# Kernel optimization log

Measured on AMD Instinct MI355X. Metric: run time of the kernel, lower is better.

## Reference

```python
import jax, jax.numpy as jnp
import numpy as np

H = 128          # h_dim
N_NODES = 100000
N_EDGES = 1600000
N_GRAPHS = 256
EPS_BN = 1e-5


def setup_inputs() -> dict:
    key = jax.random.key(0)
    ks = jax.random.split(key, 12)
    x = jax.random.normal(ks[0], (N_NODES, 4), dtype=jnp.float32)
    edge_index = jax.random.randint(ks[1], (2, N_EDGES), 0, N_NODES, dtype=jnp.int64)
    batch = jnp.sort(jax.random.randint(ks[2], (N_NODES,), 0, N_GRAPHS, dtype=jnp.int64))
    # Linear weights (xavier-ish scale), stored as [in, out]
    W1 = jax.random.normal(ks[3], (4, H), dtype=jnp.float32) * (1.0 / np.sqrt(4))
    W2 = jax.random.normal(ks[4], (H, H), dtype=jnp.float32) * (1.0 / np.sqrt(H))
    W3 = jax.random.normal(ks[5], (H, H), dtype=jnp.float32) * (1.0 / np.sqrt(H))
    Wfc = jax.random.normal(ks[6], (H, 1), dtype=jnp.float32) * (1.0 / np.sqrt(H))
    def bn_params(k):
        k1, k2, k3, k4 = jax.random.split(k, 4)
        gamma = 1.0 + 0.1 * jax.random.normal(k1, (H,), dtype=jnp.float32)
        beta = 0.1 * jax.random.normal(k2, (H,), dtype=jnp.float32)
        mean = 0.1 * jax.random.normal(k3, (H,), dtype=jnp.float32)
        var = 1.0 + 0.1 * jax.random.uniform(k4, (H,), dtype=jnp.float32)
        return gamma, beta, mean, var
    g1, b1, m1, v1 = bn_params(ks[7])
    g2, b2, m2, v2 = bn_params(ks[8])
    g3, b3, m3, v3 = bn_params(ks[9])
    return {
        "x": x, "edge_index": edge_index, "batch": batch,
        "W1": W1, "g1": g1, "b1": b1, "m1": m1, "v1": v1,
        "W2": W2, "g2": g2, "b2": b2, "m2": m2, "v2": v2,
        "W3": W3, "g3": g3, "b3": b3, "m3": m3, "v3": v3,
        "Wfc": Wfc,
    }


def _gin_layer(h, src, dst, W, gamma, beta, mean, var):
    # GINConv with eps=0: mlp(x + sum_{j in N(i)} x_j)
    aggr = jax.ops.segment_sum(h[src], dst, num_segments=N_NODES)
    z = (h + aggr) @ W                                  # Linear(bias=False)
    z = (z - mean) * (gamma / jnp.sqrt(var + EPS_BN)) + beta  # BatchNorm1d (eval)
    return jax.nn.relu(z)


def reference(x, edge_index, batch,
              W1, g1, b1, m1, v1,
              W2, g2, b2, m2, v2,
              W3, g3, b3, m3, v3,
              Wfc):
    src, dst = edge_index[0], edge_index[1]
    h = _gin_layer(x, src, dst, W1, g1, b1, m1, v1)
    h = _gin_layer(h, src, dst, W2, g2, b2, m2, v2)
    h = _gin_layer(h, src, dst, W3, g3, b3, m3, v3)
    # dropout: identity in eval mode
    sums = jax.ops.segment_sum(h, batch, num_segments=N_GRAPHS)      # [G, H]
    cnts = jax.ops.segment_sum(jnp.ones((N_NODES, 1), h.dtype), batch,
                               num_segments=N_GRAPHS)                # [G, 1]
    pooled = sums / jnp.maximum(cnts, 1.0)
    return jax.nn.sigmoid(pooled @ Wfc)                               # [G, 1]
```

## Files before the change

kernel.cpp:

```cpp
#include <hip/hip_runtime.h>
#include <hip/hip_fp8.h>
#include <math.h>

#define N_NODES 100000
#define N_EDGES 1600000
#define N_GRAPHS 256
#define H 128
#define EPS_BN 1e-5f
#define ELLW 64

#define PSZ 256
#define PSH 8
#define P_PART 391
#define BLD_NBLK 200
#define EPT 32
#define EPB_A (256 * EPT)

typedef unsigned int uint;
typedef unsigned short ushort;
typedef __attribute__((ext_vector_type(8))) short bf16x8;
typedef __attribute__((ext_vector_type(4))) float f32x4;
typedef __attribute__((ext_vector_type(2))) float f32x2;
typedef __attribute__((ext_vector_type(4))) int i32x4;

__device__ __forceinline__ uint f2bf_bits(float x) {
    uint u = __float_as_uint(x);
    return (u + 0x7fffu + ((u >> 16) & 1u)) >> 16;
}
__device__ __forceinline__ uint pack_bf2(float a, float b) {
    return f2bf_bits(a) | (f2bf_bits(b) << 16);
}

__device__ __forceinline__ unsigned char f32_to_fp8(float x) {
#if __has_builtin(__builtin_amdgcn_cvt_pk_fp8_f32)
    int v = __builtin_amdgcn_cvt_pk_fp8_f32(x, 0.0f, 0, false);
    return (unsigned char)(v & 0xff);
#else
    __hip_fp8_e4m3 q(x);
    return (unsigned char)q.__x;
#endif
}
__device__ __forceinline__ f32x4 fp8x4_to_f32x4(uint v) {
    f32x4 r;
#if __has_builtin(__builtin_amdgcn_cvt_pk_f32_fp8)
    f32x2 lo = __builtin_amdgcn_cvt_pk_f32_fp8((int)v, false);
    f32x2 hi = __builtin_amdgcn_cvt_pk_f32_fp8((int)v, true);
    r.x = lo.x; r.y = lo.y; r.z = hi.x; r.w = hi.y;
#else
    __hip_fp8_e4m3 a, b, c, d;
    a.__x = (unsigned char)(v & 0xff);
    b.__x = (unsigned char)((v >> 8) & 0xff);
    c.__x = (unsigned char)((v >> 16) & 0xff);
    d.__x = (unsigned char)((v >> 24) & 0xff);
    r.x = (float)a; r.y = (float)b; r.z = (float)c; r.w = (float)d;
#endif
    return r;
}

__global__ __launch_bounds__(256) void k_hist(const int* __restrict__ dst,
                                              int* __restrict__ hist,
                                              const int* __restrict__ batch,
                                              int* __restrict__ gstart,
                                              const float* __restrict__ W2,
                                              ushort* __restrict__ Wpk2,
                                              const float* __restrict__ W3,
                                              ushort* __restrict__ Wpk3,
                                              float* __restrict__ Gz) {
    __shared__ int h[P_PART];
    int b = blockIdx.x;
    if (b < BLD_NBLK) {
        for (int i = threadIdx.x; i < P_PART; i += 256) h[i] = 0;
        __syncthreads();
        int base = b * EPB_A + threadIdx.x * EPT;
        #pragma unroll
        for (int j = 0; j < EPT / 4; j++) {
            int e = base + j * 4;
            if (e + 4 <= N_EDGES) {
                i32x4 d = __builtin_nontemporal_load((const i32x4*)&dst[e]);
                atomicAdd(&h[d.x >> PSH], 1);
                atomicAdd(&h[d.y >> PSH], 1);
                atomicAdd(&h[d.z >> PSH], 1);
                atomicAdd(&h[d.w >> PSH], 1);
            }
        }
        __syncthreads();
        for (int i = threadIdx.x; i < P_PART; i += 256)
            hist[b * P_PART + i] = h[i];
        return;
    }
    if (b < 592) {
        int n = (b - 200) * 256 + threadIdx.x;
        if (n >= N_NODES) return;
        int g = batch[n];
        int gp = (n == 0) ? -1 : batch[n - 1];
        for (int gr = gp + 1; gr <= g; gr++) gstart[gr] = n;
        if (n == N_NODES - 1) {
            for (int gr = g + 1; gr <= N_GRAPHS; gr++) gstart[gr] = N_NODES;
        }
        return;
    }
    if (b >= 608) {
        if (threadIdx.x < N_GRAPHS) Gz[threadIdx.x] = 0.0f;
        return;
    }
    const float* W = (b < 600) ? W2 : W3;
    ushort* Wpk = (b < 600) ? Wpk2 : Wpk3;
    int t = ((b < 600) ? (b - 592) : (b - 600)) * 256 + threadIdx.x;
    int lane = t & 63, nt = (t >> 6) & 7, kt = t >> 9;
    int n = nt * 16 + (lane & 15);
    int kbase = kt * 32 + (lane >> 4) * 8;
    ushort v[8];
    #pragma unroll
    for (int j = 0; j < 8; j++)
        v[j] = (ushort)f2bf_bits(W[(size_t)(kbase + j) * H + n]);
    uint4 pk;
    pk.x = (uint)v[0] | ((uint)v[1] << 16);
    pk.y = (uint)v[2] | ((uint)v[3] << 16);
    pk.z = (uint)v[4] | ((uint)v[5] << 16);
    pk.w = (uint)v[6] | ((uint)v[7] << 16);
    *(uint4*)&Wpk[(size_t)t * 8] = pk;
}

__global__ __launch_bounds__(256) void k_scan_a(const int* __restrict__ hist,
                                                int* __restrict__ offs,
                                                int* __restrict__ tot) {
    __shared__ int lds[256];
    int p = blockIdx.x;
    int t = threadIdx.x;
    int v = (t < BLD_NBLK) ? hist[t * P_PART + p] : 0;
    lds[t] = v;
    __syncthreads();
    for (int off = 1; off < 256; off <<= 1) {
        int tmp = (t >= off) ? lds[t - off] : 0;
        __syncthreads();
        lds[t] += tmp;
        __syncthreads();
    }
    if (t < BLD_NBLK) offs[t * P_PART + p] = lds[t] - v;
    if (t == 255) tot[p] = lds[255];
}

__global__ void k_scan_b(const int* __restrict__ tot, int* __restrict__ parr) {
    __shared__ int lds[512];
    int p = threadIdx.x;
    int v = (p < P_PART) ? tot[p] : 0;
    lds[p] = v;
    __syncthreads();
    for (int off = 1; off < 512; off <<= 1) {
        int tmp = (p >= off) ? lds[p - off] : 0;
        __syncthreads();
        lds[p] += tmp;
        __syncthreads();
    }
    if (p < P_PART) parr[p] = lds[p] - v;
    if (p == 0) parr[P_PART] = N_EDGES;
}

__global__ __launch_bounds__(256) void k_scatter(const int* __restrict__ src,
                                                 const int* __restrict__ dst,
                                                 const int* __restrict__ offs,
                                                 const int* __restrict__ parr,
                                                 uint* __restrict__ ebuf) {
    __shared__ int lofs[P_PART];
    for (int i = threadIdx.x; i < P_PART; i += 256)
        lofs[i] = offs[blockIdx.x * P_PART + i] + parr[i];
    __syncthreads();
    int base = blockIdx.x * EPB_A + threadIdx.x * EPT;
    #pragma unroll
    for (int j = 0; j < EPT / 4; j++) {
        int e = base + j * 4;
        if (e + 4 <= N_EDGES) {
            i32x4 d = __builtin_nontemporal_load((const i32x4*)&dst[e]);
            i32x4 s = __builtin_nontemporal_load((const i32x4*)&src[e]);
            #pragma unroll
            for (int k = 0; k < 4; k++) {
                int dk = (k == 0) ? d.x : (k == 1) ? d.y : (k == 2) ? d.z : d.w;
                int sk = (k == 0) ? s.x : (k == 1) ? s.y : (k == 2) ? s.z : s.w;
                int pos = atomicAdd(&lofs[dk >> PSH], 1);
                ebuf[pos] = (uint)sk | ((uint)(dk & (PSZ - 1)) << 24);
            }
        }
    }
}

__global__ __launch_bounds__(256) void k_build(const uint* __restrict__ ebuf,
                                               const int* __restrict__ parr,
                                               int* __restrict__ cnt,
                                               int* __restrict__ ell) {
    __shared__ int lc[PSZ];
    int p = blockIdx.x;
    for (int i = threadIdx.x; i < PSZ; i += 256) lc[i] = 0;
    __syncthreads();
    int e0 = parr[p], e1 = parr[p + 1];
    for (int i = e0 + threadIdx.x; i < e1; i += 256) {
        uint v = __builtin_nontemporal_load(&ebuf[i]);
        int dl = (int)(v >> 24);
        int slot = atomicAdd(&lc[dl], 1);
        if (slot < ELLW)
            ell[(size_t)(p * PSZ + dl) * ELLW + slot] = (int)(v & 0x00FFFFFFu);
    }
    __syncthreads();
    int nb = p * PSZ;
    for (int i = threadIdx.x; i < PSZ; i += 256) {
        int n = nb + i;
        if (n < N_NODES) cnt[n] = lc[i];
    }
}

__global__ __launch_bounds__(256) void k_layer1(
    const float* __restrict__ x, const int* __restrict__ cnt,
    const int* __restrict__ ell, const float* __restrict__ W1,
    const float* __restrict__ gamma, const float* __restrict__ beta,
    const float* __restrict__ mean, const float* __restrict__ var,
    uint* __restrict__ Hf8) {
    __shared__ float scs[128], shs[128];
    int tid = threadIdx.x;
    if (tid < 128) {
        float sc = gamma[tid] * rsqrtf(var[tid] + EPS_BN);
        scs[tid] = sc;
        shs[tid] = beta[tid] - mean[tid] * sc;
    }
    __syncthreads();
    int lane = tid & 63, wave = tid >> 6;
    int sub = lane >> 4, m = lane & 15;
    int n = blockIdx.x * 16 + wave * 4 + sub;
    if (n >= N_NODES) return;
    int cn = cnt[n]; if (cn > ELLW) cn = ELLW;
    const int* row = &ell[(size_t)n * ELLW];
    float4 acc = {0.f, 0.f, 0.f, 0.f};
    for (int e = m; e < cn; e += 16) {
        float4 v = *(const float4*)&x[(size_t)row[e] * 4];
        acc.x += v.x; acc.y += v.y; acc.z += v.z; acc.w += v.w;
    }
    #pragma unroll
    for (int off = 8; off > 0; off >>= 1) {
        acc.x += __shfl_down(acc.x, off, 16);
        acc.y += __shfl_down(acc.y, off, 16);
        acc.z += __shfl_down(acc.z, off, 16);
        acc.w += __shfl_down(acc.w, off, 16);
    }
    int src = lane & 48;
    float4 xs = *(const float4*)&x[(size_t)n * 4];
    float uu[4];
    uu[0] = __shfl(acc.x, src, 64) + xs.x;
    uu[1] = __shfl(acc.y, src, 64) + xs.y;
    uu[2] = __shfl(acc.z, src, 64) + xs.z;
    uu[3] = __shfl(acc.w, src, 64) + xs.w;
    int j0 = m * 8;
    float z[8] = {0.f, 0.f, 0.f, 0.f, 0.f, 0.f, 0.f, 0.f};
    #pragma unroll
    for (int k = 0; k < 4; k++) {
        float4 wa = *(const float4*)&W1[k * H + j0];
        float4 wb = *(const float4*)&W1[k * H + j0 + 4];
        z[0] += uu[k] * wa.x; z[1] += uu[k] * wa.y;
        z[2] += uu[k] * wa.z; z[3] += uu[k] * wa.w;
        z[4] += uu[k] * wb.x; z[5] += uu[k] * wb.y;
        z[6] += uu[k] * wb.z; z[7] += uu[k] * wb.w;
    }
    #pragma unroll
    for (int i = 0; i < 8; i++)
        z[i] = fmaxf(z[i] * scs[j0 + i] + shs[j0 + i], 0.0f);
    uint2 q;
    q.x = (uint)f32_to_fp8(z[0]) | ((uint)f32_to_fp8(z[1]) << 8)
        | ((uint)f32_to_fp8(z[2]) << 16) | ((uint)f32_to_fp8(z[3]) << 24);
    q.y = (uint)f32_to_fp8(z[4]) | ((uint)f32_to_fp8(z[5]) << 8)
        | ((uint)f32_to_fp8(z[6]) << 16) | ((uint)f32_to_fp8(z[7]) << 24);
    *(uint2*)&Hf8[(size_t)n * 32 + m * 2] = q;
}

__global__ __launch_bounds__(256) void k_aggr128(
    const uint* __restrict__ Hf8, const int* __restrict__ cnt,
    const int* __restrict__ ell, uint* __restrict__ Ubf) {
    int t = blockIdx.x * 256 + threadIdx.x;
    int n = t >> 6, lane = t & 63;
    if (n >= N_NODES) return;
    int half = lane >> 5, c4 = lane & 31;
    float a0 = 0.f, a1 = 0.f, a2 = 0.f, a3 = 0.f;
    int cn = cnt[n]; if (cn > ELLW) cn = ELLW;
    const int* row = &ell[(size_t)n * ELLW];
    int e = half;
    for (; e + 14 < cn; e += 16) {
        int s0 = row[e + 0], s1 = row[e + 2], s2 = row[e + 4], s3 = row[e + 6];
        int s4 = row[e + 8], s5 = row[e + 10], s6 = row[e + 12], s7 = row[e + 14];
        uint p0 = Hf8[(size_t)s0 * 32 + c4];
        uint p1 = Hf8[(size_t)s1 * 32 + c4];
        uint p2 = Hf8[(size_t)s2 * 32 + c4];
        uint p3 = Hf8[(size_t)s3 * 32 + c4];
        uint p4 = Hf8[(size_t)s4 * 32 + c4];
        uint p5 = Hf8[(size_t)s5 * 32 + c4];
        uint p6 = Hf8[(size_t)s6 * 32 + c4];
        uint p7 = Hf8[(size_t)s7 * 32 + c4];
        f32x4 f0 = fp8x4_to_f32x4(p0), f1 = fp8x4_to_f32x4(p1);
        f32x4 f2 = fp8x4_to_f32x4(p2), f3 = fp8x4_to_f32x4(p3);
        f32x4 f4 = fp8x4_to_f32x4(p4), f5 = fp8x4_to_f32x4(p5);
        f32x4 f6 = fp8x4_to_f32x4(p6), f7 = fp8x4_to_f32x4(p7);
        a0 += (f0.x + f1.x + f2.x + f3.x) + (f4.x + f5.x + f6.x + f7.x);
        a1 += (f0.y + f1.y + f2.y + f3.y) + (f4.y + f5.y + f6.y + f7.y);
        a2 += (f0.z + f1.z + f2.z + f3.z) + (f4.z + f5.z + f6.z + f7.z);
        a3 += (f0.w + f1.w + f2.w + f3.w) + (f4.w + f5.w + f6.w + f7.w);
    }
    for (; e + 6 < cn; e += 8) {
        int s0 = row[e + 0], s1 = row[e + 2], s2 = row[e + 4], s3 = row[e + 6];
        uint p0 = Hf8[(size_t)s0 * 32 + c4];
        uint p1 = Hf8[(size_t)s1 * 32 + c4];
        uint p2 = Hf8[(size_t)s2 * 32 + c4];
        uint p3 = Hf8[(size_t)s3 * 32 + c4];
        f32x4 f0 = fp8x4_to_f32x4(p0), f1 = fp8x4_to_f32x4(p1);
        f32x4 f2 = fp8x4_to_f32x4(p2), f3 = fp8x4_to_f32x4(p3);
        a0 += f0.x + f1.x + f2.x + f3.x;
        a1 += f0.y + f1.y + f2.y + f3.y;
        a2 += f0.z + f1.z + f2.z + f3.z;
        a3 += f0.w + f1.w + f2.w + f3.w;
    }
    for (; e < cn; e += 2) {
        f32x4 f = fp8x4_to_f32x4(Hf8[(size_t)row[e] * 32 + c4]);
        a0 += f.x; a1 += f.y; a2 += f.z; a3 += f.w;
    }
    a0 += __shfl_down(a0, 32, 64);
    a1 += __shfl_down(a1, 32, 64);
    a2 += __shfl_down(a2, 32, 64);
    a3 += __shfl_down(a3, 32, 64);
    if (half == 0) {
        f32x4 sf = fp8x4_to_f32x4(Hf8[(size_t)n * 32 + c4]);
        a0 += sf.x; a1 += sf.y; a2 += sf.z; a3 += sf.w;
        uint2 ov; ov.x = pack_bf2(a0, a1); ov.y = pack_bf2(a2, a3);
        *(uint2*)&Ubf[(size_t)n * 64 + c4 * 2] = ov;
    }
}

__global__ __launch_bounds__(256) void k_gemm_mfma(
    const uint* __restrict__ Ubf, const uint* __restrict__ Wpk,
    const float* __restrict__ gamma, const float* __restrict__ beta,
    const float* __restrict__ mean, const float* __restrict__ var,
    unsigned char* __restrict__ Hf8,
    const int* __restrict__ batch, const float* __restrict__ Wfc,
    float* __restrict__ Gz, int mode) {
    __shared__ uint lds_u[64 * 68];
    __shared__ float wfc[128];
    __shared__ int bb[64];
    __shared__ float sblk[64];
    int tid = threadIdx.x;
    int row0 = blockIdx.x * 64;
    if (mode == 2) {
        if (tid < 128) wfc[tid] = Wfc[tid];
        if (tid < 64) {
            int rr = row0 + tid;
            bb[tid] = (rr < N_NODES) ? batch[rr] : -1;
        }
    }
    #pragma unroll
    for (int it = 0; it < 4; it++) {
        int r = it * 16 + (tid >> 4);
        int c = (tid & 15) * 4;
        int gr = row0 + r; if (gr >= N_NODES) gr = N_NODES - 1;
        uint4 v = *(const uint4*)&Ubf[(size_t)gr * 64 + c];
        *(uint4*)&lds_u[r * 68 + c] = v;
    }
    __syncthreads();

    int wave = tid >> 6, lane = tid & 63;
    int m = lane & 15, quad = lane >> 4;
    bf16x8 a[4];
    #pragma unroll
    for (int kt = 0; kt < 4; kt++)
        a[kt] = *(const bf16x8*)&lds_u[(wave * 16 + m) * 68 + kt * 16 + quad * 4];

    f32x4 acc[8];
    #pragma unroll
    for (int nt = 0; nt < 8; nt++) acc[nt] = (f32x4){0.f, 0.f, 0.f, 0.f};

    #pragma unroll
    for (int nt = 0; nt < 8; nt++) {
        #pragma unroll
        for (int kt = 0; kt < 4; kt++) {
            bf16x8 b = *(const bf16x8*)&Wpk[((size_t)(kt * 8 + nt) * 64 + lane) * 4];
            acc[nt] = __builtin_amdgcn_mfma_f32_16x16x32_bf16(a[kt], b, acc[nt], 0, 0, 0);
        }
    }

    if (mode == 1) {
        #pragma unroll
        for (int nt = 0; nt < 8; nt++) {
            int col = nt * 16 + m;
            float sc = gamma[col] * rsqrtf(var[col] + EPS_BN);
            float sh = beta[col] - mean[col] * sc;
            #pragma unroll
            for (int r = 0; r < 4; r++) {
                int row = row0 + wave * 16 + quad * 4 + r;
                float z = fmaxf(acc[nt][r] * sc + sh, 0.0f);
                uint b8 = (uint)f32_to_fp8(z);
                uint b8n = __shfl_down(b8, 1, 64);
                if ((m & 1) == 0 && row < N_NODES) {
                    *(ushort*)&Hf8[(size_t)row * 128 + col] =
                        (ushort)(b8 | (b8n << 8));
                }
            }
        }
    } else {
        float pr[4] = {0.f, 0.f, 0.f, 0.f};
        #pragma unroll
        for (int nt = 0; nt < 8; nt++) {
            int col = nt * 16 + m;
            float sc = gamma[col] * rsqrtf(var[col] + EPS_BN);
            float sh = beta[col] - mean[col] * sc;
            float wf = wfc[col];
            #pragma unroll
            for (int r = 0; r < 4; r++) {
                float z = fmaxf(acc[nt][r] * sc + sh, 0.0f);
                pr[r] += z * wf;
            }
        }
        #pragma unroll
        for (int r = 0; r < 4; r++) {
            float p = pr[r];
            p += __shfl_down(p, 8, 16);
            p += __shfl_down(p, 4, 16);
            p += __shfl_down(p, 2, 16);
            p += __shfl_down(p, 1, 16);
            if (m == 0) sblk[wave * 16 + quad * 4 + r] = p;
        }
        __syncthreads();
        if (tid == 0) {
            int i = 0;
            while (i < 64 && row0 + i < N_NODES) {
                int g = bb[i];
                float s = 0.0f;
                while (i < 64 && row0 + i < N_NODES && bb[i] == g) {
                    s += sblk[i]; i++;
                }
                atomicAdd(&Gz[g], s);
            }
        }
    }
}

__global__ void k_fc(const float* __restrict__ Gz, const int* __restrict__ gstart,
                     float* __restrict__ out) {
    int g = threadIdx.x;
    if (g < N_GRAPHS) {
        int c = gstart[g + 1] - gstart[g];
        float z = Gz[g] / fmaxf((float)c, 1.0f);
        out[g] = 1.0f / (1.0f + expf(-z));
    }
}

extern "C" void kernel_launch(void* const* d_in, const int* in_sizes, int n_in,
                              void* d_out, int out_size, void* d_ws, size_t ws_size,
                              hipStream_t stream) {
    const float* x     = (const float*)d_in[0];
    const int*   ei    = (const int*)d_in[1];
    const int*   batch = (const int*)d_in[2];
    const float* W1    = (const float*)d_in[3];
    const float* g1    = (const float*)d_in[4];
    const float* b1    = (const float*)d_in[5];
    const float* m1    = (const float*)d_in[6];
    const float* v1    = (const float*)d_in[7];
    const float* W2    = (const float*)d_in[8];
    const float* g2    = (const float*)d_in[9];
    const float* b2    = (const float*)d_in[10];
    const float* m2    = (const float*)d_in[11];
    const float* v2    = (const float*)d_in[12];
    const float* W3    = (const float*)d_in[13];
    const float* g3    = (const float*)d_in[14];
    const float* b3    = (const float*)d_in[15];
    const float* m3    = (const float*)d_in[16];
    const float* v3    = (const float*)d_in[17];
    const float* Wfc   = (const float*)d_in[18];
    float* out = (float*)d_out;

    const int* srcp = ei;
    const int* dstp = ei + N_EDGES;

    uint* Ubf  = (uint*)d_ws;
    uint* Hf8a = Ubf + (size_t)N_NODES * 64;
    uint* Hf8b = Hf8a + (size_t)N_NODES * 32;
    int* cnt   = (int*)(Hf8b + (size_t)N_NODES * 32);
    int* ell   = cnt + N_NODES;
    int* gstart = ell + (size_t)N_NODES * ELLW;
    ushort* Wpk2 = (ushort*)(gstart + 260);
    ushort* Wpk3 = Wpk2 + 16384;
    int* hist  = (int*)(Wpk3 + 16384);
    int* offs  = hist + BLD_NBLK * P_PART;
    int* parr  = offs + BLD_NBLK * P_PART;
    int* tot   = parr + 400;
    float* Gz  = (float*)(tot + 400);
    uint* ebuf = (uint*)Ubf;

    k_hist<<<609, 256, 0, stream>>>(dstp, hist, batch, gstart, W2, Wpk2, W3, Wpk3, Gz);
    k_scan_a<<<P_PART, 256, 0, stream>>>(hist, offs, tot);
    k_scan_b<<<1, 512, 0, stream>>>(tot, parr);
    k_scatter<<<BLD_NBLK, 256, 0, stream>>>(srcp, dstp, offs, parr, ebuf);
    k_build<<<P_PART, 256, 0, stream>>>(ebuf, parr, cnt, ell);

    k_layer1<<<(N_NODES + 15) / 16, 256, 0, stream>>>(
        x, cnt, ell, W1, g1, b1, m1, v1, Hf8a);
    k_aggr128<<<(N_NODES * 64 + 255) / 256, 256, 0, stream>>>(Hf8a, cnt, ell, Ubf);
    k_gemm_mfma<<<(N_NODES + 63) / 64, 256, 0, stream>>>(
        Ubf, (const uint*)Wpk2, g2, b2, m2, v2, (unsigned char*)Hf8b,
        batch, Wfc, Gz, 1);
    k_aggr128<<<(N_NODES * 64 + 255) / 256, 256, 0, stream>>>(Hf8b, cnt, ell, Ubf);
    k_gemm_mfma<<<(N_NODES + 63) / 64, 256, 0, stream>>>(
        Ubf, (const uint*)Wpk3, g3, b3, m3, v3, (unsigned char*)Hf8a,
        batch, Wfc, Gz, 2);
    k_fc<<<1, 256, 0, stream>>>(Gz, gstart, out);
}
```

Measured before the change: 310.6 us.

## Fold partition scan into scatter/build and widen aggregation loads to 8 bytes

```diff
diff --git a/kernel.cpp b/kernel.cpp
--- a/kernel.cpp
+++ b/kernel.cpp
@@ -140,32 +140,34 @@
     if (t == 255) tot[p] = lds[255];
 }
 
-__global__ void k_scan_b(const int* __restrict__ tot, int* __restrict__ parr) {
-    __shared__ int lds[512];
-    int p = threadIdx.x;
-    int v = (p < P_PART) ? tot[p] : 0;
-    lds[p] = v;
-    __syncthreads();
-    for (int off = 1; off < 512; off <<= 1) {
-        int tmp = (p >= off) ? lds[p - off] : 0;
-        __syncthreads();
-        lds[p] += tmp;
-        __syncthreads();
-    }
-    if (p < P_PART) parr[p] = lds[p] - v;
-    if (p == 0) parr[P_PART] = N_EDGES;
-}
-
 __global__ __launch_bounds__(256) void k_scatter(const int* __restrict__ src,
                                                  const int* __restrict__ dst,
                                                  const int* __restrict__ offs,
-                                                 const int* __restrict__ parr,
+                                                 const int* __restrict__ tot,
                                                  uint* __restrict__ ebuf) {
+    __shared__ int sparr[P_PART];
     __shared__ int lofs[P_PART];
-    for (int i = threadIdx.x; i < P_PART; i += 256)
-        lofs[i] = offs[blockIdx.x * P_PART + i] + parr[i];
-    __syncthreads();
-    int base = blockIdx.x * EPB_A + threadIdx.x * EPT;
+    int tid = threadIdx.x;
+    if (tid < 64) {
+        int running = 0;
+        for (int base = 0; base < P_PART; base += 64) {
+            int idx = base + tid;
+            int v = (idx < P_PART) ? tot[idx] : 0;
+            int s = v;
+            #pragma unroll
+            for (int off = 1; off < 64; off <<= 1) {
+                int u = __shfl_up(s, off, 64);
+                if (tid >= off) s += u;
+            }
+            if (idx < P_PART) sparr[idx] = running + s - v;
+            running += __shfl(s, 63, 64);
+        }
+    }
+    __syncthreads();
+    for (int i = tid; i < P_PART; i += 256)
+        lofs[i] = offs[blockIdx.x * P_PART + i] + sparr[i];
+    __syncthreads();
+    int base = blockIdx.x * EPB_A + tid * EPT;
     #pragma unroll
     for (int j = 0; j < EPT / 4; j++) {
         int e = base + j * 4;
@@ -184,15 +186,25 @@
 }
 
 __global__ __launch_bounds__(256) void k_build(const uint* __restrict__ ebuf,
-                                               const int* __restrict__ parr,
+                                               const int* __restrict__ tot,
                                                int* __restrict__ cnt,
                                                int* __restrict__ ell) {
     __shared__ int lc[PSZ];
+    __shared__ int red[256];
     int p = blockIdx.x;
-    for (int i = threadIdx.x; i < PSZ; i += 256) lc[i] = 0;
-    __syncthreads();
-    int e0 = parr[p], e1 = parr[p + 1];
-    for (int i = e0 + threadIdx.x; i < e1; i += 256) {
+    int tid = threadIdx.x;
+    int psum = 0;
+    for (int i = tid; i < p; i += 256) psum += tot[i];
+    red[tid] = psum;
+    for (int i = tid; i < PSZ; i += 256) lc[i] = 0;
+    __syncthreads();
+    for (int off = 128; off > 0; off >>= 1) {
+        if (tid < off) red[tid] += red[tid + off];
+        __syncthreads();
+    }
+    int e0 = red[0];
+    int e1 = e0 + tot[p];
+    for (int i = e0 + tid; i < e1; i += 256) {
         uint v = __builtin_nontemporal_load(&ebuf[i]);
         int dl = (int)(v >> 24);
         int slot = atomicAdd(&lc[dl], 1);
@@ -201,7 +213,7 @@
     }
     __syncthreads();
     int nb = p * PSZ;
-    for (int i = threadIdx.x; i < PSZ; i += 256) {
+    for (int i = tid; i < PSZ; i += 256) {
         int n = nb + i;
         if (n < N_NODES) cnt[n] = lc[i];
     }
@@ -269,62 +281,59 @@
 }
 
 __global__ __launch_bounds__(256) void k_aggr128(
-    const uint* __restrict__ Hf8, const int* __restrict__ cnt,
+    const uint2* __restrict__ Hf8, const int* __restrict__ cnt,
     const int* __restrict__ ell, uint* __restrict__ Ubf) {
     int t = blockIdx.x * 256 + threadIdx.x;
     int n = t >> 6, lane = t & 63;
     if (n >= N_NODES) return;
-    int half = lane >> 5, c4 = lane & 31;
+    int g = lane >> 4, c = lane & 15;
     float a0 = 0.f, a1 = 0.f, a2 = 0.f, a3 = 0.f;
+    float a4 = 0.f, a5 = 0.f, a6 = 0.f, a7 = 0.f;
     int cn = cnt[n]; if (cn > ELLW) cn = ELLW;
     const int* row = &ell[(size_t)n * ELLW];
-    int e = half;
-    for (; e + 14 < cn; e += 16) {
-        int s0 = row[e + 0], s1 = row[e + 2], s2 = row[e + 4], s3 = row[e + 6];
-        int s4 = row[e + 8], s5 = row[e + 10], s6 = row[e + 12], s7 = row[e + 14];
-        uint p0 = Hf8[(size_t)s0 * 32 + c4];
-        uint p1 = Hf8[(size_t)s1 * 32 + c4];
-        uint p2 = Hf8[(size_t)s2 * 32 + c4];
-        uint p3 = Hf8[(size_t)s3 * 32 + c4];
-        uint p4 = Hf8[(size_t)s4 * 32 + c4];
-        uint p5 = Hf8[(size_t)s5 * 32 + c4];
-        uint p6 = Hf8[(size_t)s6 * 32 + c4];
-        uint p7 = Hf8[(size_t)s7 * 32 + c4];
-        f32x4 f0 = fp8x4_to_f32x4(p0), f1 = fp8x4_to_f32x4(p1);
-        f32x4 f2 = fp8x4_to_f32x4(p2), f3 = fp8x4_to_f32x4(p3);
-        f32x4 f4 = fp8x4_to_f32x4(p4), f5 = fp8x4_to_f32x4(p5);
-        f32x4 f6 = fp8x4_to_f32x4(p6), f7 = fp8x4_to_f32x4(p7);
-        a0 += (f0.x + f1.x + f2.x + f3.x) + (f4.x + f5.x + f6.x + f7.x);
-        a1 += (f0.y + f1.y + f2.y + f3.y) + (f4.y + f5.y + f6.y + f7.y);
-        a2 += (f0.z + f1.z + f2.z + f3.z) + (f4.z + f5.z + f6.z + f7.z);
-        a3 += (f0.w + f1.w + f2.w + f3.w) + (f4.w + f5.w + f6.w + f7.w);
-    }
-    for (; e + 6 < cn; e += 8) {
-        int s0 = row[e + 0], s1 = row[e + 2], s2 = row[e + 4], s3 = row[e + 6];
-        uint p0 = Hf8[(size_t)s0 * 32 + c4];
-        uint p1 = Hf8[(size_t)s1 * 32 + c4];
-        uint p2 = Hf8[(size_t)s2 * 32 + c4];
-        uint p3 = Hf8[(size_t)s3 * 32 + c4];
-        f32x4 f0 = fp8x4_to_f32x4(p0), f1 = fp8x4_to_f32x4(p1);
-        f32x4 f2 = fp8x4_to_f32x4(p2), f3 = fp8x4_to_f32x4(p3);
-        a0 += f0.x + f1.x + f2.x + f3.x;
-        a1 += f0.y + f1.y + f2.y + f3.y;
-        a2 += f0.z + f1.z + f2.z + f3.z;
-        a3 += f0.w + f1.w + f2.w + f3.w;
-    }
-    for (; e < cn; e += 2) {
-        f32x4 f = fp8x4_to_f32x4(Hf8[(size_t)row[e] * 32 + c4]);
-        a0 += f.x; a1 += f.y; a2 += f.z; a3 += f.w;
-    }
-    a0 += __shfl_down(a0, 32, 64);
-    a1 += __shfl_down(a1, 32, 64);
-    a2 += __shfl_down(a2, 32, 64);
-    a3 += __shfl_down(a3, 32, 64);
-    if (half == 0) {
-        f32x4 sf = fp8x4_to_f32x4(Hf8[(size_t)n * 32 + c4]);
-        a0 += sf.x; a1 += sf.y; a2 += sf.z; a3 += sf.w;
-        uint2 ov; ov.x = pack_bf2(a0, a1); ov.y = pack_bf2(a2, a3);
-        *(uint2*)&Ubf[(size_t)n * 64 + c4 * 2] = ov;
+    int e = g;
+    for (; e + 12 < cn; e += 16) {
+        int s0 = row[e], s1 = row[e + 4], s2 = row[e + 8], s3 = row[e + 12];
+        uint2 p0 = Hf8[(size_t)s0 * 16 + c];
+        uint2 p1 = Hf8[(size_t)s1 * 16 + c];
+        uint2 p2 = Hf8[(size_t)s2 * 16 + c];
+        uint2 p3 = Hf8[(size_t)s3 * 16 + c];
+        f32x4 l0 = fp8x4_to_f32x4(p0.x), h0 = fp8x4_to_f32x4(p0.y);
+        f32x4 l1 = fp8x4_to_f32x4(p1.x), h1 = fp8x4_to_f32x4(p1.y);
+        f32x4 l2 = fp8x4_to_f32x4(p2.x), h2 = fp8x4_to_f32x4(p2.y);
+        f32x4 l3 = fp8x4_to_f32x4(p3.x), h3 = fp8x4_to_f32x4(p3.y);
+        a0 += l0.x + l1.x + l2.x + l3.x;
+        a1 += l0.y + l1.y + l2.y + l3.y;
+        a2 += l0.z + l1.z + l2.z + l3.z;
+        a3 += l0.w + l1.w + l2.w + l3.w;
+        a4 += h0.x + h1.x + h2.x + h3.x;
+        a5 += h0.y + h1.y + h2.y + h3.y;
+        a6 += h0.z + h1.z + h2.z + h3.z;
+        a7 += h0.w + h1.w + h2.w + h3.w;
+    }
+    for (; e < cn; e += 4) {
+        uint2 p = Hf8[(size_t)row[e] * 16 + c];
+        f32x4 lo = fp8x4_to_f32x4(p.x), hi = fp8x4_to_f32x4(p.y);
+        a0 += lo.x; a1 += lo.y; a2 += lo.z; a3 += lo.w;
+        a4 += hi.x; a5 += hi.y; a6 += hi.z; a7 += hi.w;
+    }
+    a0 += __shfl_down(a0, 32, 64); a1 += __shfl_down(a1, 32, 64);
+    a2 += __shfl_down(a2, 32, 64); a3 += __shfl_down(a3, 32, 64);
+    a4 += __shfl_down(a4, 32, 64); a5 += __shfl_down(a5, 32, 64);
+    a6 += __shfl_down(a6, 32, 64); a7 += __shfl_down(a7, 32, 64);
+    a0 += __shfl_down(a0, 16, 64); a1 += __shfl_down(a1, 16, 64);
+    a2 += __shfl_down(a2, 16, 64); a3 += __shfl_down(a3, 16, 64);
+    a4 += __shfl_down(a4, 16, 64); a5 += __shfl_down(a5, 16, 64);
+    a6 += __shfl_down(a6, 16, 64); a7 += __shfl_down(a7, 16, 64);
+    if (g == 0) {
+        uint2 sp = Hf8[(size_t)n * 16 + c];
+        f32x4 slo = fp8x4_to_f32x4(sp.x), shi = fp8x4_to_f32x4(sp.y);
+        a0 += slo.x; a1 += slo.y; a2 += slo.z; a3 += slo.w;
+        a4 += shi.x; a5 += shi.y; a6 += shi.z; a7 += shi.w;
+        uint4 ov;
+        ov.x = pack_bf2(a0, a1); ov.y = pack_bf2(a2, a3);
+        ov.z = pack_bf2(a4, a5); ov.w = pack_bf2(a6, a7);
+        *(uint4*)&Ubf[(size_t)n * 64 + c * 4] = ov;
     }
 }
 
@@ -387,12 +396,9 @@
             #pragma unroll
             for (int r = 0; r < 4; r++) {
                 int row = row0 + wave * 16 + quad * 4 + r;
-                float z = fmaxf(acc[nt][r] * sc + sh, 0.0f);
-                uint b8 = (uint)f32_to_fp8(z);
-                uint b8n = __shfl_down(b8, 1, 64);
-                if ((m & 1) == 0 && row < N_NODES) {
-                    *(ushort*)&Hf8[(size_t)row * 128 + col] =
-                        (ushort)(b8 | (b8n << 8));
+                if (row < N_NODES) {
+                    float z = fmaxf(acc[nt][r] * sc + sh, 0.0f);
+                    Hf8[(size_t)row * 128 + col] = f32_to_fp8(z);
                 }
             }
         }
@@ -481,24 +487,24 @@
     ushort* Wpk3 = Wpk2 + 16384;
     int* hist  = (int*)(Wpk3 + 16384);
     int* offs  = hist + BLD_NBLK * P_PART;
-    int* parr  = offs + BLD_NBLK * P_PART;
-    int* tot   = parr + 400;
+    int* tot   = offs + BLD_NBLK * P_PART;
     float* Gz  = (float*)(tot + 400);
     uint* ebuf = (uint*)Ubf;
 
     k_hist<<<609, 256, 0, stream>>>(dstp, hist, batch, gstart, W2, Wpk2, W3, Wpk3, Gz);
     k_scan_a<<<P_PART, 256, 0, stream>>>(hist, offs, tot);
-    k_scan_b<<<1, 512, 0, stream>>>(tot, parr);
-    k_scatter<<<BLD_NBLK, 256, 0, stream>>>(srcp, dstp, offs, parr, ebuf);
-    k_build<<<P_PART, 256, 0, stream>>>(ebuf, parr, cnt, ell);
+    k_scatter<<<BLD_NBLK, 256, 0, stream>>>(srcp, dstp, offs, tot, ebuf);
+    k_build<<<P_PART, 256, 0, stream>>>(ebuf, tot, cnt, ell);
 
     k_layer1<<<(N_NODES + 15) / 16, 256, 0, stream>>>(
         x, cnt, ell, W1, g1, b1, m1, v1, Hf8a);
-    k_aggr128<<<(N_NODES * 64 + 255) / 256, 256, 0, stream>>>(Hf8a, cnt, ell, Ubf);
+    k_aggr128<<<(N_NODES * 64 + 255) / 256, 256, 0, stream>>>(
+        (const uint2*)Hf8a, cnt, ell, Ubf);
     k_gemm_mfma<<<(N_NODES + 63) / 64, 256, 0, stream>>>(
         Ubf, (const uint*)Wpk2, g2, b2, m2, v2, (unsigned char*)Hf8b,
         batch, Wfc, Gz, 1);
-    k_aggr128<<<(N_NODES * 64 + 255) / 256, 256, 0, stream>>>(Hf8b, cnt, ell, Ubf);
+    k_aggr128<<<(N_NODES * 64 + 255) / 256, 256, 0, stream>>>(
+        (const uint2*)Hf8b, cnt, ell, Ubf);
     k_gemm_mfma<<<(N_NODES + 63) / 64, 256, 0, stream>>>(
         Ubf, (const uint*)Wpk3, g3, b3, m3, v3, (unsigned char*)Hf8a,
         batch, Wfc, Gz, 2);
```

Result: no change. 307.6 us (-0.9%).
